# Optimization experiments

Measured on AMD Instinct MI355X. Metric: run time of the kernel, lower is better.

## Reference

```python
import jax, jax.numpy as jnp
import numpy as np

N_NODES = 50000


def _gcn_conv(x, src, dst, W, b, num_nodes):
    """PyG GCNConv: out = D^{-1/2}(A+I)D^{-1/2} (x @ W) + b, self-loops added."""
    h = x @ W  # [N, out]
    # degrees over edges incl. self-loops (src/dst already include self-loops)
    ones = jnp.ones(src.shape[0], dtype=h.dtype)
    deg = jax.ops.segment_sum(ones, dst, num_segments=num_nodes)
    dinv = jnp.where(deg > 0, jax.lax.rsqrt(deg), 0.0)
    norm = dinv[src] * dinv[dst]  # [E]
    msgs = h[src] * norm[:, None]  # [E, out] gather (memory-bound)
    out = jax.ops.segment_sum(msgs, dst, num_segments=num_nodes)
    return out + b


def setup_inputs() -> dict:
    key = jax.random.key(0)
    ks = jax.random.split(key, 8)
    in_c, h2, h1, out_c = 256, 256, 128, 128
    x = jax.random.normal(ks[0], (N_NODES, in_c), dtype=jnp.float32)
    edge_index = jax.random.randint(ks[1], (2, 800000), 0, N_NODES, dtype=jnp.int64)
    def glorot(k, fi, fo):
        s = float(np.sqrt(6.0 / (fi + fo)))
        return jax.random.uniform(k, (fi, fo), jnp.float32, -s, s)
    return {
        "x": x,
        "edge_index": edge_index,
        "W1": glorot(ks[2], in_c, h2), "b1": jnp.zeros((h2,), jnp.float32),
        "W2": glorot(ks[3], h2, h1), "b2": jnp.zeros((h1,), jnp.float32),
        "W3": glorot(ks[4], h1, out_c), "b3": jnp.zeros((out_c,), jnp.float32),
    }


def reference(x, edge_index, W1, b1, W2, b2, W3, b3):
    n = x.shape[0]
    loops = jnp.arange(n, dtype=edge_index.dtype)
    src = jnp.concatenate([edge_index[0], loops])
    dst = jnp.concatenate([edge_index[1], loops])
    # dropout is a no-op in eval mode (training=False)
    h1 = jax.nn.relu(_gcn_conv(x, src, dst, W1, b1, n))
    h2 = jax.nn.relu(_gcn_conv(h1, src, dst, W2, b2, n))
    h3 = jax.nn.relu(_gcn_conv(h2, src, dst, W3, b3, n))
    return jnp.concatenate([h1, h2, h3], axis=1)
```

## Files before the change

### kernel.cpp

```cpp
#include <hip/hip_runtime.h>

typedef __attribute__((ext_vector_type(8))) short bfrag8;
typedef __attribute__((ext_vector_type(4))) float f32x4v;
typedef __attribute__((ext_vector_type(4))) int   i32x4v;

__device__ inline short f2bf(float f) {
    unsigned u = __builtin_bit_cast(unsigned, f);
    u = (u + 0x7FFFu + ((u >> 16) & 1u)) >> 16;
    return (short)u;
}
__device__ inline float bf2f(short s) {
    unsigned u = ((unsigned)(unsigned short)s) << 16;
    return __builtin_bit_cast(float, u);
}
__device__ inline int pack2(short lo, short hi) {
    return (int)(((unsigned)(unsigned short)lo) | (((unsigned)(unsigned short)hi) << 16));
}
__device__ inline int pad16i(int v) { return (v + 15) & ~15; }


__global__ void block_sum_kernel(const int* __restrict__ deg, int n, int* __restrict__ bsums) {
    int i = blockIdx.x * 256 + threadIdx.x;
    int v = (i < n) ? pad16i(deg[i] + 1) : 0;
#pragma unroll
    for (int off = 32; off > 0; off >>= 1) v += __shfl_down(v, off);
    __shared__ int wsum[4];
    int lane = threadIdx.x & 63, w = threadIdx.x >> 6;
    if (lane == 0) wsum[w] = v;
    __syncthreads();
    if (threadIdx.x == 0) bsums[blockIdx.x] = wsum[0] + wsum[1] + wsum[2] + wsum[3];
}

__global__ void scan_final_kernel(const int* __restrict__ deg, int n, int B,
                                  const int* __restrict__ bsums,
                                  int* __restrict__ offs, int* __restrict__ cursor,
                                  float* __restrict__ dinv, int* __restrict__ csr) {
    __shared__ int sb[256];
    __shared__ int s[256];
    int tid = threadIdx.x;
    sb[tid] = (tid < B) ? bsums[tid] : 0;
    __syncthreads();
    for (int off = 1; off < 256; off <<= 1) {
        int t = (tid >= off) ? sb[tid - off] : 0;
        __syncthreads();
        sb[tid] += t;
        __syncthreads();
    }
    int myBase = (blockIdx.x == 0) ? 0 : sb[blockIdx.x - 1];
    int total = sb[255];
    int i = blockIdx.x * 256 + tid;
    int vt = (i < n) ? deg[i] + 1 : 0;
    int pv = (i < n) ? pad16i(vt) : 0;
    s[tid] = pv;
    __syncthreads();
    for (int off = 1; off < 256; off <<= 1) {
        int t = (tid >= off) ? s[tid - off] : 0;
        __syncthreads();
        s[tid] += t;
        __syncthreads();
    }
    if (i < n) {
        int excl = s[tid] - pv + myBase;
        offs[i] = excl;
        csr[excl] = i;
        cursor[i] = excl + 1;
        for (int p = excl + vt; p < excl + pv; ++p) csr[p] = n;
        dinv[i] = rsqrtf((float)vt);
    } else if (i < gridDim.x * 256) {
        dinv[i] = 0.f;
    }
    if (blockIdx.x == 0 && tid == 0) offs[n] = total;
}


__global__ void prep_kernel(const int* __restrict__ dst, int E, int* __restrict__ deg,
                            const float* __restrict__ x, short* __restrict__ xb,
                            int total8, int totalp8,
                            const float* __restrict__ W1, short* __restrict__ Wt1,
                            const float* __restrict__ W2, short* __restrict__ Wt2,
                            const float* __restrict__ W3, short* __restrict__ Wt3) {
    int g = blockIdx.x * blockDim.x + threadIdx.x;
    if (g < E) {
        atomicAdd(&deg[dst[g]], 1);
        return;
    }
    int i = g - E;
    if (i < total8) {
        const float4* p = (const float4*)(x + (size_t)i * 8);
        float4 v0 = p[0], v1 = p[1];
        int4 w = make_int4(pack2(f2bf(v0.x), f2bf(v0.y)), pack2(f2bf(v0.z), f2bf(v0.w)),
                           pack2(f2bf(v1.x), f2bf(v1.y)), pack2(f2bf(v1.z), f2bf(v1.w)));
        *(int4*)(xb + (size_t)i * 8) = w;
    } else if (i < totalp8) {
        *(int4*)(xb + (size_t)i * 8) = make_int4(0, 0, 0, 0);
    } else {
        int j = i - totalp8;
        if (j < 65536) {
            int k = j >> 8, c = j & 255;
            Wt1[c * 256 + k] = f2bf(W1[j]);
        } else if (j < 65536 + 32768) {
            int m = j - 65536;
            int k = m >> 7, c = m & 127;
            Wt2[c * 256 + k] = f2bf(W2[m]);
        } else if (j < 65536 + 32768 + 16384) {
            int m = j - 65536 - 32768;
            int k = m >> 7, c = m & 127;
            Wt3[c * 128 + k] = f2bf(W3[m]);
        }
    }
}


template<int K>
__device__ __forceinline__ void gemm_body(
        const short* __restrict__ A, const short* __restrict__ Bt,
        const float* __restrict__ dinv, short* __restrict__ Tout, int ldt,
        int bx, int by, char* bsb) {
    const int tid = threadIdx.x;
    const int lane = tid & 63;
    const int wid = tid >> 6;
    const int l15 = lane & 15;
    const int quad = lane >> 4;
    const int q8 = quad * 8;
    const int bn = by * 128;
    const int row0 = bx * 256 + wid * 64;

    {
        constexpr int TOT16 = 128 * K / 8;
#pragma unroll
        for (int i = tid; i < TOT16; i += 256) {
            int r = i / (K / 8);
            int c = (i % (K / 8)) * 8;
            int byteoff = (r * K + c) * 2;
            byteoff ^= (r & 7) << 4;
            *(int4*)(bsb + byteoff) = *(const int4*)&Bt[(size_t)(bn + r) * K + c];
        }
    }
    __syncthreads();

    f32x4v acc[4][8];
#pragma unroll
    for (int i = 0; i < 4; ++i)
#pragma unroll
        for (int j = 0; j < 8; ++j) acc[i][j] = (f32x4v){0.f, 0.f, 0.f, 0.f};

    const short* aBase = A + (size_t)(row0 + l15) * K + q8;

#pragma unroll
    for (int ks = 0; ks < K / 32; ++ks) {
        bfrag8 af[4], bf[8];
#pragma unroll
        for (int mt = 0; mt < 4; ++mt)
            af[mt] = *(const bfrag8*)(aBase + (size_t)mt * 16 * K + ks * 32);
#pragma unroll
        for (int nt = 0; nt < 8; ++nt) {
            int r = nt * 16 + l15;
            int byteoff = (r * K + ks * 32 + q8) * 2;
            byteoff ^= (r & 7) << 4;
            bf[nt] = *(const bfrag8*)(bsb + byteoff);
        }
#pragma unroll
        for (int mt = 0; mt < 4; ++mt)
#pragma unroll
            for (int nt = 0; nt < 8; ++nt)
                acc[mt][nt] = __builtin_amdgcn_mfma_f32_16x16x32_bf16(af[mt], bf[nt], acc[mt][nt], 0, 0, 0);
    }

#pragma unroll
    for (int mt = 0; mt < 4; ++mt) {
#pragma unroll
        for (int r = 0; r < 4; ++r) {
            int grow = row0 + mt * 16 + quad * 4 + r;
            float di = dinv[grow];
            short* outp = Tout + (size_t)grow * ldt + bn + l15;
#pragma unroll
            for (int nt = 0; nt < 8; ++nt)
                outp[nt * 16] = f2bf(acc[mt][nt][r] * di);
        }
    }
}

template<int K>
__global__ __launch_bounds__(256, 2) void gemm_csr_kernel(
        const short* __restrict__ A, const short* __restrict__ Bt,
        const float* __restrict__ dinv, short* __restrict__ Tout, int ldt, int tilesX,
        const int* __restrict__ src, const int* __restrict__ dst, int E,
        int* __restrict__ cursor, int* __restrict__ csr, int csrBlocks) {
    __shared__ short Bs[128 * K];
    if ((int)blockIdx.x < csrBlocks) {
        int e = blockIdx.x * 256 + threadIdx.x;
        if (e < E) {
            int d = dst[e];
            int p = atomicAdd(&cursor[d], 1);
            csr[p] = src[e];
        }
        return;
    }
    int tile = blockIdx.x - csrBlocks;
    gemm_body<K>(A, Bt, dinv, Tout, ldt, tile % tilesX, tile / tilesX, (char*)Bs);
}


__global__ __launch_bounds__(256) void aggmm256_kernel(
        const short* __restrict__ t1, const float* __restrict__ dinv,
        const int* __restrict__ offs, const int* __restrict__ csr,
        const float* __restrict__ bias, const short* __restrict__ Wt2,
        float* __restrict__ out, short* __restrict__ t2, int n) {
    __shared__ short h1s[64 * 256];
    char* hsb = (char*)h1s;
    const int tid = threadIdx.x;
    const int lane = tid & 63;
    const int wid = tid >> 6;
    const int hl = lane & 31;
    const int sub = lane >> 5;
    const int base = blockIdx.x * 64;
    const short* gb = t1 + hl * 8;

    for (int i = 0; i < 16; ++i) {
        int row = wid * 16 + i;
        int node = base + row;
        int lbyte = (row * 512 + hl * 16) ^ ((row & 7) << 4);
        if (node < n) {
            float acc[8];
#pragma unroll
            for (int v = 0; v < 8; ++v) acc[v] = 0.f;
            int beg = offs[node], end = offs[node + 1];
            for (int e = beg + sub; e < end; e += 16) {
                int s[8];
#pragma unroll
                for (int j = 0; j < 8; ++j) s[j] = __builtin_nontemporal_load(csr + e + 2 * j);
                bfrag8 r[8];
#pragma unroll
                for (int j = 0; j < 8; ++j) r[j] = *(const bfrag8*)(gb + (size_t)s[j] * 256);
#pragma unroll
                for (int j = 0; j < 8; ++j)
#pragma unroll
                    for (int v = 0; v < 8; ++v) acc[v] += bf2f(r[j][v]);
            }
#pragma unroll
            for (int v = 0; v < 8; ++v) acc[v] += __shfl_xor(acc[v], 32);
            if (sub == 0) {
                float di = dinv[node];
                float res[8];
#pragma unroll
                for (int v = 0; v < 8; ++v)
                    res[v] = fmaxf(fmaf(di, acc[v], bias[hl * 8 + v]), 0.f);
                float* op = out + (size_t)node * 512 + hl * 8;
                f32x4v w0 = {res[0], res[1], res[2], res[3]};
                f32x4v w1 = {res[4], res[5], res[6], res[7]};
                __builtin_nontemporal_store(w0, (f32x4v*)op);
                __builtin_nontemporal_store(w1, (f32x4v*)(op + 4));
                i32x4v w = {pack2(f2bf(res[0]), f2bf(res[1])), pack2(f2bf(res[2]), f2bf(res[3])),
                            pack2(f2bf(res[4]), f2bf(res[5])), pack2(f2bf(res[6]), f2bf(res[7]))};
                *(i32x4v*)(hsb + lbyte) = w;
            }
        } else if (sub == 0) {
            i32x4v z = {0, 0, 0, 0};
            *(i32x4v*)(hsb + lbyte) = z;
        }
    }
    __syncthreads();

    const int l15 = lane & 15;
    const int quad = lane >> 4;
    const int q8 = quad * 8;
    const int wn0 = wid * 32;
    f32x4v acc2[4][2];
#pragma unroll
    for (int i = 0; i < 4; ++i)
#pragma unroll
        for (int j = 0; j < 2; ++j) acc2[i][j] = (f32x4v){0.f, 0.f, 0.f, 0.f};
#pragma unroll
    for (int ks = 0; ks < 8; ++ks) {
        bfrag8 af[4], bf[2];
#pragma unroll
        for (int mt = 0; mt < 4; ++mt) {
            int row = mt * 16 + l15;
            int byteoff = (row * 512 + ks * 64 + q8 * 2) ^ ((row & 7) << 4);
            af[mt] = *(const bfrag8*)(hsb + byteoff);
        }
#pragma unroll
        for (int nt = 0; nt < 2; ++nt) {
            int col = wn0 + nt * 16 + l15;
            bf[nt] = *(const bfrag8*)(Wt2 + (size_t)col * 256 + ks * 32 + q8);
        }
#pragma unroll
        for (int mt = 0; mt < 4; ++mt)
#pragma unroll
            for (int nt = 0; nt < 2; ++nt)
                acc2[mt][nt] = __builtin_amdgcn_mfma_f32_16x16x32_bf16(af[mt], bf[nt], acc2[mt][nt], 0, 0, 0);
    }
#pragma unroll
    for (int mt = 0; mt < 4; ++mt) {
#pragma unroll
        for (int r = 0; r < 4; ++r) {
            int grow = base + mt * 16 + quad * 4 + r;
            float di = dinv[grow];
            short* tp = t2 + (size_t)grow * 128 + wn0 + l15;
#pragma unroll
            for (int nt = 0; nt < 2; ++nt)
                tp[nt * 16] = f2bf(acc2[mt][nt][r] * di);
        }
    }
}


__global__ __launch_bounds__(256) void aggmm128_kernel(
        const short* __restrict__ t2, const float* __restrict__ dinv,
        const int* __restrict__ offs, const int* __restrict__ csr,
        const float* __restrict__ bias, const short* __restrict__ Wt3,
        float* __restrict__ out, short* __restrict__ t3, int n) {
    __shared__ short h2s[64 * 128];
    char* hsb = (char*)h2s;
    const int tid = threadIdx.x;
    const int lane = tid & 63;
    const int wid = tid >> 6;
    const int ch = lane & 15;
    const int sub = lane >> 4;
    const int base = blockIdx.x * 64;
    const short* gb = t2 + ch * 8;

    for (int i = 0; i < 16; ++i) {
        int row = wid * 16 + i;
        int node = base + row;
        int lbyte = (row * 256 + ch * 16) ^ ((row & 7) << 4);
        if (node < n) {
            float acc[8];
#pragma unroll
            for (int v = 0; v < 8; ++v) acc[v] = 0.f;
            int beg = offs[node], end = offs[node + 1];
            int e = beg + sub;
            for (; e + 16 < end; e += 32) {
                int s[8];
#pragma unroll
                for (int j = 0; j < 8; ++j) s[j] = __builtin_nontemporal_load(csr + e + 4 * j);
                bfrag8 r[8];
#pragma unroll
                for (int j = 0; j < 8; ++j) r[j] = *(const bfrag8*)(gb + (size_t)s[j] * 128);
#pragma unroll
                for (int j = 0; j < 8; ++j)
#pragma unroll
                    for (int v = 0; v < 8; ++v) acc[v] += bf2f(r[j][v]);
            }
            if (e < end) {
                int s[4];
#pragma unroll
                for (int j = 0; j < 4; ++j) s[j] = __builtin_nontemporal_load(csr + e + 4 * j);
                bfrag8 r[4];
#pragma unroll
                for (int j = 0; j < 4; ++j) r[j] = *(const bfrag8*)(gb + (size_t)s[j] * 128);
#pragma unroll
                for (int j = 0; j < 4; ++j)
#pragma unroll
                    for (int v = 0; v < 8; ++v) acc[v] += bf2f(r[j][v]);
            }
#pragma unroll
            for (int v = 0; v < 8; ++v) {
                acc[v] += __shfl_xor(acc[v], 16);
                acc[v] += __shfl_xor(acc[v], 32);
            }
            if (sub == 0) {
                float di = dinv[node];
                float res[8];
#pragma unroll
                for (int v = 0; v < 8; ++v)
                    res[v] = fmaxf(fmaf(di, acc[v], bias[ch * 8 + v]), 0.f);
                float* op = out + (size_t)node * 512 + 256 + ch * 8;
                f32x4v w0 = {res[0], res[1], res[2], res[3]};
                f32x4v w1 = {res[4], res[5], res[6], res[7]};
                __builtin_nontemporal_store(w0, (f32x4v*)op);
                __builtin_nontemporal_store(w1, (f32x4v*)(op + 4));
                i32x4v w = {pack2(f2bf(res[0]), f2bf(res[1])), pack2(f2bf(res[2]), f2bf(res[3])),
                            pack2(f2bf(res[4]), f2bf(res[5])), pack2(f2bf(res[6]), f2bf(res[7]))};
                *(i32x4v*)(hsb + lbyte) = w;
            }
        } else if (sub == 0) {
            i32x4v z = {0, 0, 0, 0};
            *(i32x4v*)(hsb + lbyte) = z;
        }
    }
    __syncthreads();

    const int l15 = lane & 15;
    const int quad = lane >> 4;
    const int q8 = quad * 8;
    const int wn0 = wid * 32;
    f32x4v acc2[4][2];
#pragma unroll
    for (int i = 0; i < 4; ++i)
#pragma unroll
        for (int j = 0; j < 2; ++j) acc2[i][j] = (f32x4v){0.f, 0.f, 0.f, 0.f};
#pragma unroll
    for (int ks = 0; ks < 4; ++ks) {
        bfrag8 af[4], bf[2];
#pragma unroll
        for (int mt = 0; mt < 4; ++mt) {
            int row = mt * 16 + l15;
            int byteoff = (row * 256 + ks * 64 + q8 * 2) ^ ((row & 7) << 4);
            af[mt] = *(const bfrag8*)(hsb + byteoff);
        }
#pragma unroll
        for (int nt = 0; nt < 2; ++nt) {
            int col = wn0 + nt * 16 + l15;
            bf[nt] = *(const bfrag8*)(Wt3 + (size_t)col * 128 + ks * 32 + q8);
        }
#pragma unroll
        for (int mt = 0; mt < 4; ++mt)
#pragma unroll
            for (int nt = 0; nt < 2; ++nt)
                acc2[mt][nt] = __builtin_amdgcn_mfma_f32_16x16x32_bf16(af[mt], bf[nt], acc2[mt][nt], 0, 0, 0);
    }
#pragma unroll
    for (int mt = 0; mt < 4; ++mt) {
#pragma unroll
        for (int r = 0; r < 4; ++r) {
            int grow = base + mt * 16 + quad * 4 + r;
            float di = dinv[grow];
            short* tp = t3 + (size_t)grow * 128 + wn0 + l15;
#pragma unroll
            for (int nt = 0; nt < 2; ++nt)
                tp[nt * 16] = f2bf(acc2[mt][nt][r] * di);
        }
    }
}


__global__ __launch_bounds__(256) void agg128_kernel(
        const short* __restrict__ hn, const float* __restrict__ dinv,
        const int* __restrict__ offs, const int* __restrict__ csr,
        const float* __restrict__ bias, float* __restrict__ out,
        int coloff, int n) {
    int node = blockIdx.x * 4 + (threadIdx.x >> 6);
    if (node >= n) return;
    int lane = threadIdx.x & 63;
    int ch = lane & 15;
    int sub = lane >> 4;
    const short* base = hn + ch * 8;

    float acc[8];
#pragma unroll
    for (int v = 0; v < 8; ++v) acc[v] = 0.f;

    int beg = offs[node], end = offs[node + 1];
    int e = beg + sub;
    for (; e + 16 < end; e += 32) {
        int s[8];
#pragma unroll
        for (int j = 0; j < 8; ++j) s[j] = __builtin_nontemporal_load(csr + e + 4 * j);
        bfrag8 r[8];
#pragma unroll
        for (int j = 0; j < 8; ++j) r[j] = *(const bfrag8*)(base + (size_t)s[j] * 128);
#pragma unroll
        for (int j = 0; j < 8; ++j)
#pragma unroll
            for (int v = 0; v < 8; ++v) acc[v] += bf2f(r[j][v]);
    }
    if (e < end) {
        int s[4];
#pragma unroll
        for (int j = 0; j < 4; ++j) s[j] = __builtin_nontemporal_load(csr + e + 4 * j);
        bfrag8 r[4];
#pragma unroll
        for (int j = 0; j < 4; ++j) r[j] = *(const bfrag8*)(base + (size_t)s[j] * 128);
#pragma unroll
        for (int j = 0; j < 4; ++j)
#pragma unroll
            for (int v = 0; v < 8; ++v) acc[v] += bf2f(r[j][v]);
    }

#pragma unroll
    for (int v = 0; v < 8; ++v) {
        acc[v] += __shfl_xor(acc[v], 16);
        acc[v] += __shfl_xor(acc[v], 32);
    }

    if (sub == 0) {
        float di = dinv[node];
        float res[8];
#pragma unroll
        for (int v = 0; v < 8; ++v)
            res[v] = fmaxf(fmaf(di, acc[v], bias[ch * 8 + v]), 0.f);
        float* op = out + (size_t)node * 512 + coloff + ch * 8;
        f32x4v w0 = {res[0], res[1], res[2], res[3]};
        f32x4v w1 = {res[4], res[5], res[6], res[7]};
        __builtin_nontemporal_store(w0, (f32x4v*)op);
        __builtin_nontemporal_store(w1, (f32x4v*)(op + 4));
    }
}


extern "C" void kernel_launch(void* const* d_in, const int* in_sizes, int n_in,
                              void* d_out, int out_size, void* d_ws, size_t ws_size,
                              hipStream_t stream) {
    const float* x  = (const float*)d_in[0];
    const int*   ei = (const int*)d_in[1];
    const float* W1 = (const float*)d_in[2];
    const float* b1 = (const float*)d_in[3];
    const float* W2 = (const float*)d_in[4];
    const float* b2 = (const float*)d_in[5];
    const float* W3 = (const float*)d_in[6];
    const float* b3 = (const float*)d_in[7];

    const int IN_C = 256, H2 = 256, H1 = 128, OUT_C = 128;
    int n = in_sizes[0] / IN_C;
    int E = in_sizes[1] / 2;
    const int* src = ei;
    const int* dst = ei + E;

    int sb = (n + 255) / 256;
    int npad = sb * 256;

    char* ws = (char*)d_ws;
    auto carve = [&](size_t bytes) { char* p = ws; ws += (bytes + 255) & ~(size_t)255; return p; };
    int*   deg    = (int*)  carve((size_t)n * 4);
    int*   offs   = (int*)  carve(((size_t)n + 1) * 4);
    int*   cursor = (int*)  carve((size_t)n * 4);
    float* dinv   = (float*)carve((size_t)npad * 4);
    int*   csr    = (int*)  carve(((size_t)E + 16 * (size_t)n) * 4);
    int*   bsums  = (int*)  carve(256 * 4);
    short* Wt1    = (short*)carve((size_t)IN_C * H2 * 2);
    short* Wt2    = (short*)carve((size_t)H2 * H1 * 2);
    short* Wt3    = (short*)carve((size_t)H1 * OUT_C * 2);
    short* t1     = (short*)carve((size_t)npad * 256 * 2);
    short* t2     = (short*)carve((size_t)npad * 128 * 2);
    short* t3     = (short*)carve((size_t)npad * 128 * 2);
    short* xb     = (short*)carve((size_t)npad * 256 * 2);

    float* out = (float*)d_out;
    int nblk = (n + 255) / 256;

    hipMemsetAsync(deg, 0, (size_t)n * sizeof(int), stream);

    int total8 = n * IN_C / 8;
    int totalp8 = npad * IN_C / 8;
    int prepTot = E + totalp8 + 65536 + 32768 + 16384;
    prep_kernel<<<(prepTot + 255) / 256, 256, 0, stream>>>(
        dst, E, deg, x, xb, total8, totalp8, W1, Wt1, W2, Wt2, W3, Wt3);

    block_sum_kernel<<<nblk, 256, 0, stream>>>(deg, n, bsums);
    scan_final_kernel<<<nblk, 256, 0, stream>>>(deg, n, nblk, bsums, offs, cursor, dinv, csr);

    int csrBlocks = (E + 255) / 256;
    int gemmTiles = sb * (H2 / 128);
    gemm_csr_kernel<256><<<csrBlocks + gemmTiles, 256, 0, stream>>>(
        xb, Wt1, dinv, t1, H2, sb, src, dst, E, cursor, csr, csrBlocks);

    int nb64 = (n + 63) / 64;
    aggmm256_kernel<<<nb64, 256, 0, stream>>>(t1, dinv, offs, csr, b1, Wt2, out, t2, n);

    aggmm128_kernel<<<nb64, 256, 0, stream>>>(t2, dinv, offs, csr, b2, Wt3, out, t3, n);

    agg128_kernel<<<(n + 3) / 4, 256, 0, stream>>>(t3, dinv, offs, csr, b3, out, H2 + H1, n);
}
```

Baseline: 445.3 us.

## Shrink fused aggregate-GEMM blocks from 64 to 16 nodes per block

The fused aggregation+GEMM kernels now process 16 nodes per block instead of 64, each wave aggregating 4 interleaved rows and doing a single 16-row MFMA tile across its 32 output columns. This gives four times as many blocks and a quarter of the shared memory per block. The aim is better load balance across CUs and less tail imbalance from the irregular-degree gather loop. In exchange, each block reloads the full weight matrix from global memory for only 16 rows, so weight reuse drops. The grid size formula and buffer carve order also change, with xb moved before t1.

```diff
diff --git a/kernel.cpp b/kernel.cpp
--- a/kernel.cpp
+++ b/kernel.cpp
@@ -206,18 +206,19 @@
         const int* __restrict__ offs, const int* __restrict__ csr,
         const float* __restrict__ bias, const short* __restrict__ Wt2,
         float* __restrict__ out, short* __restrict__ t2, int n) {
-    __shared__ short h1s[64 * 256];
+    __shared__ short h1s[16 * 256];
     char* hsb = (char*)h1s;
     const int tid = threadIdx.x;
     const int lane = tid & 63;
     const int wid = tid >> 6;
     const int hl = lane & 31;
     const int sub = lane >> 5;
-    const int base = blockIdx.x * 64;
+    const int base = blockIdx.x * 16;
     const short* gb = t1 + hl * 8;
 
-    for (int i = 0; i < 16; ++i) {
-        int row = wid * 16 + i;
+#pragma unroll
+    for (int i = 0; i < 4; ++i) {
+        int row = wid + 4 * i;
         int node = base + row;
         int lbyte = (row * 512 + hl * 16) ^ ((row & 7) << 4);
         if (node < n) {
@@ -265,63 +266,45 @@
     const int quad = lane >> 4;
     const int q8 = quad * 8;
     const int wn0 = wid * 32;
-    f32x4v acc2[4][2];
-#pragma unroll
-    for (int i = 0; i < 4; ++i)
-#pragma unroll
-        for (int j = 0; j < 2; ++j) acc2[i][j] = (f32x4v){0.f, 0.f, 0.f, 0.f};
+    f32x4v a0 = {0.f, 0.f, 0.f, 0.f}, a1 = {0.f, 0.f, 0.f, 0.f};
 #pragma unroll
     for (int ks = 0; ks < 8; ++ks) {
-        bfrag8 af[4], bf[2];
-#pragma unroll
-        for (int mt = 0; mt < 4; ++mt) {
-            int row = mt * 16 + l15;
-            int byteoff = (row * 512 + ks * 64 + q8 * 2) ^ ((row & 7) << 4);
-            af[mt] = *(const bfrag8*)(hsb + byteoff);
-        }
-#pragma unroll
-        for (int nt = 0; nt < 2; ++nt) {
-            int col = wn0 + nt * 16 + l15;
-            bf[nt] = *(const bfrag8*)(Wt2 + (size_t)col * 256 + ks * 32 + q8);
-        }
-#pragma unroll
-        for (int mt = 0; mt < 4; ++mt)
-#pragma unroll
-            for (int nt = 0; nt < 2; ++nt)
-                acc2[mt][nt] = __builtin_amdgcn_mfma_f32_16x16x32_bf16(af[mt], bf[nt], acc2[mt][nt], 0, 0, 0);
-    }
-#pragma unroll
-    for (int mt = 0; mt < 4; ++mt) {
-#pragma unroll
-        for (int r = 0; r < 4; ++r) {
-            int grow = base + mt * 16 + quad * 4 + r;
-            float di = dinv[grow];
-            short* tp = t2 + (size_t)grow * 128 + wn0 + l15;
-#pragma unroll
-            for (int nt = 0; nt < 2; ++nt)
-                tp[nt * 16] = f2bf(acc2[mt][nt][r] * di);
-        }
+        int byteoff = (l15 * 512 + ks * 64 + q8 * 2) ^ ((l15 & 7) << 4);
+        bfrag8 af = *(const bfrag8*)(hsb + byteoff);
+        bfrag8 bf0 = *(const bfrag8*)(Wt2 + (size_t)(wn0 + l15) * 256 + ks * 32 + q8);
+        bfrag8 bf1 = *(const bfrag8*)(Wt2 + (size_t)(wn0 + 16 + l15) * 256 + ks * 32 + q8);
+        a0 = __builtin_amdgcn_mfma_f32_16x16x32_bf16(af, bf0, a0, 0, 0, 0);
+        a1 = __builtin_amdgcn_mfma_f32_16x16x32_bf16(af, bf1, a1, 0, 0, 0);
+    }
+#pragma unroll
+    for (int r = 0; r < 4; ++r) {
+        int grow = base + quad * 4 + r;
+        float di = dinv[grow];
+        short* tp = t2 + (size_t)grow * 128 + wn0 + l15;
+        tp[0]  = f2bf(a0[r] * di);
+        tp[16] = f2bf(a1[r] * di);
     }
 }
 
 
 __global__ __launch_bounds__(256) void aggmm128_kernel(
-        const short* __restrict__ t2, const float* __restrict__ dinv,
+        const short* __restrict__ t2s, const float* __restrict__ dinv,
         const int* __restrict__ offs, const int* __restrict__ csr,
         const float* __restrict__ bias, const short* __restrict__ Wt3,
         float* __restrict__ out, short* __restrict__ t3, int n) {
-    __shared__ short h2s[64 * 128];
+    __shared__ short h2s[16 * 128];
     char* hsb = (char*)h2s;
     const int tid = threadIdx.x;
     const int lane = tid & 63;
     const int wid = tid >> 6;
     const int ch = lane & 15;
     const int sub = lane >> 4;
-    const int base = blockIdx.x * 64;
-    const short* gb = t2 + ch * 8;
-
-    for (int i = 0; i < 16; ++i) {
-        int row = wid * 16 + i;
+    const int base = blockIdx.x * 16;
+    const short* gb = t2s + ch * 8;
+
+#pragma unroll
+    for (int i = 0; i < 4; ++i) {
+        int row = wid + 4 * i;
         int node = base + row;
         int lbyte = (row * 256 + ch * 16) ^ ((row & 7) << 4);
         if (node < n) {
@@ -385,42 +368,23 @@
     const int quad = lane >> 4;
     const int q8 = quad * 8;
     const int wn0 = wid * 32;
-    f32x4v acc2[4][2];
-#pragma unroll
-    for (int i = 0; i < 4; ++i)
-#pragma unroll
-        for (int j = 0; j < 2; ++j) acc2[i][j] = (f32x4v){0.f, 0.f, 0.f, 0.f};
+    f32x4v a0 = {0.f, 0.f, 0.f, 0.f}, a1 = {0.f, 0.f, 0.f, 0.f};
 #pragma unroll
     for (int ks = 0; ks < 4; ++ks) {
-        bfrag8 af[4], bf[2];
-#pragma unroll
-        for (int mt = 0; mt < 4; ++mt) {
-            int row = mt * 16 + l15;
-            int byteoff = (row * 256 + ks * 64 + q8 * 2) ^ ((row & 7) << 4);
-            af[mt] = *(const bfrag8*)(hsb + byteoff);
-        }
-#pragma unroll
-        for (int nt = 0; nt < 2; ++nt) {
-            int col = wn0 + nt * 16 + l15;
-            bf[nt] = *(const bfrag8*)(Wt3 + (size_t)col * 128 + ks * 32 + q8);
-        }
-#pragma unroll
-        for (int mt = 0; mt < 4; ++mt)
-#pragma unroll
-            for (int nt = 0; nt < 2; ++nt)
-                acc2[mt][nt] = __builtin_amdgcn_mfma_f32_16x16x32_bf16(af[mt], bf[nt], acc2[mt][nt], 0, 0, 0);
-    }
-#pragma unroll
-    for (int mt = 0; mt < 4; ++mt) {
-#pragma unroll
-        for (int r = 0; r < 4; ++r) {
-            int grow = base + mt * 16 + quad * 4 + r;
-            float di = dinv[grow];
-            short* tp = t3 + (size_t)grow * 128 + wn0 + l15;
-#pragma unroll
-            for (int nt = 0; nt < 2; ++nt)
-                tp[nt * 16] = f2bf(acc2[mt][nt][r] * di);
-        }
+        int byteoff = (l15 * 256 + ks * 64 + q8 * 2) ^ ((l15 & 7) << 4);
+        bfrag8 af = *(const bfrag8*)(hsb + byteoff);
+        bfrag8 bf0 = *(const bfrag8*)(Wt3 + (size_t)(wn0 + l15) * 128 + ks * 32 + q8);
+        bfrag8 bf1 = *(const bfrag8*)(Wt3 + (size_t)(wn0 + 16 + l15) * 128 + ks * 32 + q8);
+        a0 = __builtin_amdgcn_mfma_f32_16x16x32_bf16(af, bf0, a0, 0, 0, 0);
+        a1 = __builtin_amdgcn_mfma_f32_16x16x32_bf16(af, bf1, a1, 0, 0, 0);
+    }
+#pragma unroll
+    for (int r = 0; r < 4; ++r) {
+        int grow = base + quad * 4 + r;
+        float di = dinv[grow];
+        short* tp = t3 + (size_t)grow * 128 + wn0 + l15;
+        tp[0]  = f2bf(a0[r] * di);
+        tp[16] = f2bf(a1[r] * di);
     }
 }
 
@@ -521,10 +485,10 @@
     short* Wt1    = (short*)carve((size_t)IN_C * H2 * 2);
     short* Wt2    = (short*)carve((size_t)H2 * H1 * 2);
     short* Wt3    = (short*)carve((size_t)H1 * OUT_C * 2);
+    short* xb     = (short*)carve((size_t)npad * 256 * 2);
     short* t1     = (short*)carve((size_t)npad * 256 * 2);
     short* t2     = (short*)carve((size_t)npad * 128 * 2);
     short* t3     = (short*)carve((size_t)npad * 128 * 2);
-    short* xb     = (short*)carve((size_t)npad * 256 * 2);
 
     float* out = (float*)d_out;
     int nblk = (n + 255) / 256;
@@ -545,10 +509,10 @@
     gemm_csr_kernel<256><<<csrBlocks + gemmTiles, 256, 0, stream>>>(
         xb, Wt1, dinv, t1, H2, sb, src, dst, E, cursor, csr, csrBlocks);
 
-    int nb64 = (n + 63) / 64;
-    aggmm256_kernel<<<nb64, 256, 0, stream>>>(t1, dinv, offs, csr, b1, Wt2, out, t2, n);
-
-    aggmm128_kernel<<<nb64, 256, 0, stream>>>(t2, dinv, offs, csr, b2, Wt3, out, t3, n);
+    int nb16 = (n + 1 + 15) / 16;
+    aggmm256_kernel<<<nb16, 256, 0, stream>>>(t1, dinv, offs, csr, b1, Wt2, out, t2, n);
+
+    aggmm128_kernel<<<nb16, 256, 0, stream>>>(t2, dinv, offs, csr, b2, Wt3, out, t3, n);
 
     agg128_kernel<<<(n + 3) / 4, 256, 0, stream>>>(t3, dinv, offs, csr, b3, out, H2 + H1, n);
 }
```

Result: faster. 424.8 us (-4.6%).
